# Kernel optimization log

Measured on AMD Instinct MI355X. Metric: run time of the kernel, lower is better.

## Reference

```python
import jax, jax.numpy as jnp
import numpy as np

B, T, D, H = 2048, 200, 128, 128


def setup_inputs() -> dict:
    key = jax.random.key(0)
    k1, k2, k3, k4, k5, k6 = jax.random.split(key, 6)
    inputs = jax.random.normal(k1, (B, T, D), dtype=jnp.float32)
    att_scores = jax.random.uniform(k2, (B, T), dtype=jnp.float32)
    seq_len = jax.random.randint(k3, (B,), 0, T, dtype=jnp.int32)
    s = 1.0 / np.sqrt(D + H)
    Wg = jax.random.normal(k4, (D + H, 2 * H), dtype=jnp.float32) * s
    bg = jnp.ones((2 * H,), dtype=jnp.float32)  # TF GRU gate bias init = 1.0
    Wc = jax.random.normal(k5, (D + H, H), dtype=jnp.float32) * s
    bc = jnp.zeros((H,), dtype=jnp.float32)
    return {"inputs": inputs, "att_scores": att_scores, "seq_len": seq_len,
            "Wg": Wg, "bg": bg, "Wc": Wc, "bc": bc}


def _augru_scan(inputs, att_scores, seq_len, Wg, bg, Wc, bc):
    # time-major xs for scan
    xs = (jnp.swapaxes(inputs, 0, 1),          # [T, B, D]
          jnp.swapaxes(att_scores, 0, 1),      # [T, B]
          jnp.arange(T, dtype=jnp.int32))      # [T]
    h0 = jnp.zeros((inputs.shape[0], H), dtype=inputs.dtype)

    def step(h, x):
        x_t, a_t, t = x
        # gates: sigmoid([x, h] @ Wg + bg) -> reset r, update u
        gi = jax.nn.sigmoid(jnp.concatenate([x_t, h], axis=-1) @ Wg + bg)
        r, u = jnp.split(gi, 2, axis=-1)
        # candidate: tanh([x, r*h] @ Wc + bc)
        c = jnp.tanh(jnp.concatenate([x_t, r * h], axis=-1) @ Wc + bc)
        # attention-gated update (AUGRU): scale update gate by att score
        u = a_t[:, None] * u
        new_h = (1.0 - u) * h + u * c
        # sequence-length masking (TF _rnn_step copy_cond: time >= seq_len)
        valid = (t < seq_len)[:, None]
        out = jnp.where(valid, new_h, jnp.zeros_like(new_h))  # zero_output
        h = jnp.where(valid, new_h, h)                         # carry old state
        return h, out

    final_h, outs = jax.lax.scan(step, h0, xs)
    return jnp.swapaxes(outs, 0, 1)  # [B, T, H]


def reference(inputs, att_scores, seq_len, Wg, bg, Wc, bc):
    return _augru_scan(inputs, att_scores, seq_len, Wg, bg, Wc, bc)
```

## Files before the change

### kernel.cpp

```cpp
#include <hip/hip_runtime.h>
#include <hip/hip_bf16.h>


#define BB   2048
#define TT   200
#define DD   128
#define HH   128
#define NG   256
#define BM   8
#define SB   136
#define SF   132
#define NTH  512

typedef __attribute__((ext_vector_type(8))) __bf16 bf16x8;
typedef __attribute__((ext_vector_type(4))) float  f32x4;

#define MFMA(a, b, c) __builtin_amdgcn_mfma_f32_16x16x32_bf16((a), (b), (c), 0, 0, 0)

union bfu { __bf16 b; unsigned short u; };
__device__ __forceinline__ unsigned short f2bf(float f) { bfu c; c.b = (__bf16)f; return c.u; }
__device__ __forceinline__ __bf16 f2bfv(float f) { return (__bf16)f; }

__device__ __forceinline__ void lds_barrier() {
    __builtin_amdgcn_sched_barrier(0);
    asm volatile("s_waitcnt lgkmcnt(0)" ::: "memory");
    __builtin_amdgcn_s_barrier();
    __builtin_amdgcn_sched_barrier(0);
}

__global__ __launch_bounds__(NTH, 2)
void augru_kernel(const float* __restrict__ X,
                  const float* __restrict__ ATT,
                  const int*   __restrict__ SL,
                  const float* __restrict__ WG,
                  const float* __restrict__ BG,
                  const float* __restrict__ WC,
                  const float* __restrict__ BC,
                  float*       __restrict__ OUT)
{
    __shared__ unsigned short xb[2][16 * SB];
    __shared__ unsigned short hb[16 * SB];
    __shared__ unsigned short rh[16 * SB];
    __shared__ float hs[BM * SF];
    __shared__ float ub[BM * SF];
    __shared__ float attall[BM * TT];
    __shared__ int   slbuf[BM];

    const int tid  = threadIdx.x;
    const int wave = tid >> 6;
    const int lane = tid & 63;
    const int quad = lane >> 4;
    const int l16  = lane & 15;
    const int b0   = blockIdx.x * BM;
    const int qq   = quad & 1;
    const int top  = quad >> 1;
    const int r0   = 4 * qq + 2 * top;

    for (int i = tid; i < 2 * 16 * SB; i += NTH) xb[0][i] = 0;
    for (int i = tid; i < 16 * SB; i += NTH) hb[i] = 0;
    for (int i = tid; i < 16 * SB; i += NTH) rh[i] = 0;
    for (int i = tid; i < BM * SF; i += NTH) { hs[i] = 0.f; ub[i] = 0.f; }
    for (int i = tid; i < BM * TT; i += NTH) attall[i] = ATT[(long)b0 * TT + i];
    if (tid < BM) slbuf[tid] = SL[b0 + tid];

    const float bgv0 = BG[(2 * wave) * 16 + l16];
    const float bgv1 = BG[(2 * wave + 1) * 16 + l16];
    const float bcv  = BC[wave * 16 + l16];

    bf16x8 bgf[2][8], bcf[8];
    {
        const int nc0 = (2 * wave) * 16 + l16;
        const int nc1 = nc0 + 16;
        const int ncc = wave * 16 + l16;
        #pragma unroll
        for (int kk = 0; kk < 8; ++kk) {
            bf16x8 t0, t1, t2;
            #pragma unroll
            for (int j = 0; j < 8; ++j) {
                const int k = kk * 32 + quad * 8 + j;
                t0[j] = f2bfv(WG[k * NG + nc0]);
                t1[j] = f2bfv(WG[k * NG + nc1]);
                t2[j] = f2bfv(WC[k * HH + ncc]);
            }
            bgf[0][kk] = t0; bgf[1][kk] = t1; bcf[kk] = t2;
        }
    }
    __syncthreads();

    int tmax = 0;
    #pragma unroll
    for (int r = 0; r < BM; ++r) tmax = max(tmax, slbuf[r]);
    const int sl0 = slbuf[r0], sl1 = slbuf[r0 + 1];

    const int srow = tid >> 5;
    const int sseg = tid & 31;

    float4 xpre;
    if (tid < 256 && tmax > 0) {
        xpre = *(const float4*)&X[((long)(b0 + srow) * TT + 0) * DD + sseg * 4];
        ushort4 v; v.x = f2bf(xpre.x); v.y = f2bf(xpre.y); v.z = f2bf(xpre.z); v.w = f2bf(xpre.w);
        *(ushort4*)&xb[0][srow * SB + sseg * 4] = v;
        if (tmax > 1)
            xpre = *(const float4*)&X[((long)(b0 + srow) * TT + 1) * DD + sseg * 4];
    }
    lds_barrier();

    for (int t = 0; t < tmax; ++t) {
        const unsigned short* xc = &xb[t & 1][0];

        bf16x8 afx[4];
        #pragma unroll
        for (int kk = 0; kk < 4; ++kk)
            afx[kk] = *(const bf16x8*)&xc[l16 * SB + kk * 32 + quad * 8];

        f32x4 a0 = {0.f,0.f,0.f,0.f}, a1 = {0.f,0.f,0.f,0.f};
        f32x4 a2 = {0.f,0.f,0.f,0.f}, a3 = {0.f,0.f,0.f,0.f};
        a0 = MFMA(afx[0], bgf[0][0], a0); a1 = MFMA(afx[0], bgf[1][0], a1);
        a2 = MFMA(afx[1], bgf[0][1], a2); a3 = MFMA(afx[1], bgf[1][1], a3);
        a0 = MFMA(afx[2], bgf[0][2], a0); a1 = MFMA(afx[2], bgf[1][2], a1);
        a2 = MFMA(afx[3], bgf[0][3], a2); a3 = MFMA(afx[3], bgf[1][3], a3);
        #pragma unroll
        for (int kk = 4; kk < 8; kk += 2) {
            const bf16x8 af0 = *(const bf16x8*)&hb[l16 * SB + (kk - 4) * 32 + quad * 8];
            const bf16x8 af1 = *(const bf16x8*)&hb[l16 * SB + (kk - 3) * 32 + quad * 8];
            a0 = MFMA(af0, bgf[0][kk], a0);     a1 = MFMA(af0, bgf[1][kk], a1);
            a2 = MFMA(af1, bgf[0][kk + 1], a2); a3 = MFMA(af1, bgf[1][kk + 1], a3);
        }

        if (tid < 256 && t + 1 < tmax) {
            ushort4 v; v.x = f2bf(xpre.x); v.y = f2bf(xpre.y); v.z = f2bf(xpre.z); v.w = f2bf(xpre.w);
            *(ushort4*)&xb[(t + 1) & 1][srow * SB + sseg * 4] = v;
            if (t + 2 < tmax)
                xpre = *(const float4*)&X[((long)(b0 + srow) * TT + (t + 2)) * DD + sseg * 4];
        }

        const f32x4 g0 = a0 + a2;
        const f32x4 g1 = a1 + a3;
        float s20 = __shfl_xor(g0[2], 32, 64), s30 = __shfl_xor(g0[3], 32, 64);
        float s21 = __shfl_xor(g1[2], 32, 64), s31 = __shfl_xor(g1[3], 32, 64);
        #pragma unroll
        for (int nt = 0; nt < 2; ++nt) {
            const int colg = (2 * wave + nt) * 16 + l16;
            const float bg = nt ? bgv1 : bgv0;
            const float v0 = top ? (nt ? s21 : s20) : (nt ? g1[0] : g0[0]);
            const float v1 = top ? (nt ? s31 : s30) : (nt ? g1[1] : g0[1]);
            #pragma unroll
            for (int rr = 0; rr < 2; ++rr) {
                const int row = r0 + rr;
                const float pre = (rr ? v1 : v0) + bg;
                const float s = __builtin_amdgcn_rcpf(1.0f + __expf(-pre));
                if (wave < 4) {
                    rh[row * SB + colg] = f2bf(s * hs[row * SF + colg]);
                } else {
                    ub[row * SF + (colg - HH)] = attall[row * TT + t] * s;
                }
            }
        }
        lds_barrier();

        f32x4 c0 = {0.f,0.f,0.f,0.f}, c1 = {0.f,0.f,0.f,0.f};
        f32x4 c2 = {0.f,0.f,0.f,0.f}, c3 = {0.f,0.f,0.f,0.f};
        {
            const bf16x8 afr0 = *(const bf16x8*)&rh[l16 * SB + 0 * 32 + quad * 8];
            const bf16x8 afr1 = *(const bf16x8*)&rh[l16 * SB + 1 * 32 + quad * 8];
            const bf16x8 afr2 = *(const bf16x8*)&rh[l16 * SB + 2 * 32 + quad * 8];
            const bf16x8 afr3 = *(const bf16x8*)&rh[l16 * SB + 3 * 32 + quad * 8];
            c0 = MFMA(afx[0], bcf[0], c0); c1 = MFMA(afr0, bcf[4], c1);
            c2 = MFMA(afx[1], bcf[1], c2); c3 = MFMA(afr1, bcf[5], c3);
            c0 = MFMA(afx[2], bcf[2], c0); c1 = MFMA(afr2, bcf[6], c1);
            c2 = MFMA(afx[3], bcf[3], c2); c3 = MFMA(afr3, bcf[7], c3);
        }
        const f32x4 cc = (c0 + c2) + (c1 + c3);
        float t2 = __shfl_xor(cc[2], 32, 64), t3 = __shfl_xor(cc[3], 32, 64);

        {
            const int col = wave * 16 + l16;
            const float w0 = top ? t2 : cc[0];
            const float w1 = top ? t3 : cc[1];
            #pragma unroll
            for (int rr = 0; rr < 2; ++rr) {
                const int row = r0 + rr;
                const float xv = (rr ? w1 : w0) + bcv;
                const float e  = __expf(2.0f * xv);
                const float c  = 1.0f - 2.0f * __builtin_amdgcn_rcpf(e + 1.0f);
                const float u  = ub[row * SF + col];
                const float ho = hs[row * SF + col];
                const float nh = fmaf(u, c - ho, ho);
                const bool valid = t < (rr ? sl1 : sl0);
                const float hst = valid ? nh : ho;
                hs[row * SF + col] = hst;
                hb[row * SB + col] = f2bf(hst);
                OUT[((long)(b0 + row) * TT + t) * HH + col] = valid ? nh : 0.f;
            }
        }
        lds_barrier();
    }

    const int n4 = (TT - tmax) * (HH / 4);
    for (int r = 0; r < BM; ++r) {
        float4* p = (float4*)(OUT + ((long)(b0 + r) * TT + tmax) * HH);
        for (int i = tid; i < n4; i += NTH) p[i] = make_float4(0.f, 0.f, 0.f, 0.f);
    }
}

extern "C" void kernel_launch(void* const* d_in, const int* in_sizes, int n_in,
                              void* d_out, int out_size, void* d_ws, size_t ws_size,
                              hipStream_t stream) {
    (void)in_sizes; (void)n_in; (void)d_ws; (void)ws_size; (void)out_size;
    const float* X   = (const float*)d_in[0];
    const float* ATT = (const float*)d_in[1];
    const int*   SL  = (const int*)d_in[2];
    const float* WG  = (const float*)d_in[3];
    const float* BG  = (const float*)d_in[4];
    const float* WC  = (const float*)d_in[5];
    const float* BC  = (const float*)d_in[6];
    float*       OUT = (float*)d_out;
    hipLaunchKernelGGL(augru_kernel, dim3(BB / BM), dim3(NTH), 0, stream,
                       X, ATT, SL, WG, BG, WC, BC, OUT);
}
```

Before: 573.8 us.

## Halve block to four waves, keep hidden state and update gate in registers

The block shrinks from 8 to 4 waves. Each wave now computes both the reset and update gate columns, plus two candidate column tiles, for the same 32 hidden columns. This lets the fp32 hidden state and the attention-scaled update gate stay in registers, removing the hs/ub shared-memory round trips and their loads and stores each step. The cost is double the register-resident weight fragments per thread, a launch bound of 1 block per SIMD slot, and more serial MFMA work per wave on the recurrent critical path.

```diff
diff --git a/kernel.cpp b/kernel.cpp
--- a/kernel.cpp
+++ b/kernel.cpp
@@ -9,8 +9,7 @@
 #define NG   256
 #define BM   8
 #define SB   136
-#define SF   132
-#define NTH  512
+#define NTH  256
 
 typedef __attribute__((ext_vector_type(8))) __bf16 bf16x8;
 typedef __attribute__((ext_vector_type(4))) float  f32x4;
@@ -20,6 +19,7 @@
 union bfu { __bf16 b; unsigned short u; };
 __device__ __forceinline__ unsigned short f2bf(float f) { bfu c; c.b = (__bf16)f; return c.u; }
 __device__ __forceinline__ __bf16 f2bfv(float f) { return (__bf16)f; }
+__device__ __forceinline__ float sigm(float x) { return __builtin_amdgcn_rcpf(1.0f + __expf(-x)); }
 
 __device__ __forceinline__ void lds_barrier() {
     __builtin_amdgcn_sched_barrier(0);
@@ -28,7 +28,7 @@
     __builtin_amdgcn_sched_barrier(0);
 }
 
-__global__ __launch_bounds__(NTH, 2)
+__global__ __launch_bounds__(NTH, 1)
 void augru_kernel(const float* __restrict__ X,
                   const float* __restrict__ ATT,
                   const int*   __restrict__ SL,
@@ -41,8 +41,6 @@
     __shared__ unsigned short xb[2][16 * SB];
     __shared__ unsigned short hb[16 * SB];
     __shared__ unsigned short rh[16 * SB];
-    __shared__ float hs[BM * SF];
-    __shared__ float ub[BM * SF];
     __shared__ float attall[BM * TT];
     __shared__ int   slbuf[BM];
 
@@ -59,30 +57,32 @@
     for (int i = tid; i < 2 * 16 * SB; i += NTH) xb[0][i] = 0;
     for (int i = tid; i < 16 * SB; i += NTH) hb[i] = 0;
     for (int i = tid; i < 16 * SB; i += NTH) rh[i] = 0;
-    for (int i = tid; i < BM * SF; i += NTH) { hs[i] = 0.f; ub[i] = 0.f; }
     for (int i = tid; i < BM * TT; i += NTH) attall[i] = ATT[(long)b0 * TT + i];
     if (tid < BM) slbuf[tid] = SL[b0 + tid];
 
-    const float bgv0 = BG[(2 * wave) * 16 + l16];
-    const float bgv1 = BG[(2 * wave + 1) * 16 + l16];
-    const float bcv  = BC[wave * 16 + l16];
-
-    bf16x8 bgf[2][8], bcf[8];
+    const int c0 = wave * 32 + l16;
+    const int c1 = c0 + 16;
+    const float bgr0 = BG[c0],      bgr1 = BG[c1];
+    const float bgu0 = BG[c0 + HH], bgu1 = BG[c1 + HH];
+    const float bc0v = BC[c0],      bc1v = BC[c1];
+
+    bf16x8 bgf[4][8], bcf[2][8];
     {
-        const int nc0 = (2 * wave) * 16 + l16;
-        const int nc1 = nc0 + 16;
-        const int ncc = wave * 16 + l16;
         #pragma unroll
         for (int kk = 0; kk < 8; ++kk) {
-            bf16x8 t0, t1, t2;
+            bf16x8 t0, t1, t2, t3, t4, t5;
             #pragma unroll
             for (int j = 0; j < 8; ++j) {
                 const int k = kk * 32 + quad * 8 + j;
-                t0[j] = f2bfv(WG[k * NG + nc0]);
-                t1[j] = f2bfv(WG[k * NG + nc1]);
-                t2[j] = f2bfv(WC[k * HH + ncc]);
-            }
-            bgf[0][kk] = t0; bgf[1][kk] = t1; bcf[kk] = t2;
+                t0[j] = f2bfv(WG[k * NG + c0]);
+                t1[j] = f2bfv(WG[k * NG + c1]);
+                t2[j] = f2bfv(WG[k * NG + c0 + HH]);
+                t3[j] = f2bfv(WG[k * NG + c1 + HH]);
+                t4[j] = f2bfv(WC[k * HH + c0]);
+                t5[j] = f2bfv(WC[k * HH + c1]);
+            }
+            bgf[0][kk] = t0; bgf[1][kk] = t1; bgf[2][kk] = t2; bgf[3][kk] = t3;
+            bcf[0][kk] = t4; bcf[1][kk] = t5;
         }
     }
     __syncthreads();
@@ -92,11 +92,13 @@
     for (int r = 0; r < BM; ++r) tmax = max(tmax, slbuf[r]);
     const int sl0 = slbuf[r0], sl1 = slbuf[r0 + 1];
 
+    float h00 = 0.f, h01 = 0.f, h10 = 0.f, h11 = 0.f;
+
     const int srow = tid >> 5;
     const int sseg = tid & 31;
 
     float4 xpre;
-    if (tid < 256 && tmax > 0) {
+    if (tmax > 0) {
         xpre = *(const float4*)&X[((long)(b0 + srow) * TT + 0) * DD + sseg * 4];
         ushort4 v; v.x = f2bf(xpre.x); v.y = f2bf(xpre.y); v.z = f2bf(xpre.z); v.w = f2bf(xpre.w);
         *(ushort4*)&xb[0][srow * SB + sseg * 4] = v;
@@ -113,84 +115,127 @@
         for (int kk = 0; kk < 4; ++kk)
             afx[kk] = *(const bf16x8*)&xc[l16 * SB + kk * 32 + quad * 8];
 
+        const float at0 = attall[r0 * TT + t];
+        const float at1 = attall[(r0 + 1) * TT + t];
+
         f32x4 a0 = {0.f,0.f,0.f,0.f}, a1 = {0.f,0.f,0.f,0.f};
         f32x4 a2 = {0.f,0.f,0.f,0.f}, a3 = {0.f,0.f,0.f,0.f};
-        a0 = MFMA(afx[0], bgf[0][0], a0); a1 = MFMA(afx[0], bgf[1][0], a1);
-        a2 = MFMA(afx[1], bgf[0][1], a2); a3 = MFMA(afx[1], bgf[1][1], a3);
-        a0 = MFMA(afx[2], bgf[0][2], a0); a1 = MFMA(afx[2], bgf[1][2], a1);
-        a2 = MFMA(afx[3], bgf[0][3], a2); a3 = MFMA(afx[3], bgf[1][3], a3);
-        #pragma unroll
-        for (int kk = 4; kk < 8; kk += 2) {
-            const bf16x8 af0 = *(const bf16x8*)&hb[l16 * SB + (kk - 4) * 32 + quad * 8];
-            const bf16x8 af1 = *(const bf16x8*)&hb[l16 * SB + (kk - 3) * 32 + quad * 8];
-            a0 = MFMA(af0, bgf[0][kk], a0);     a1 = MFMA(af0, bgf[1][kk], a1);
-            a2 = MFMA(af1, bgf[0][kk + 1], a2); a3 = MFMA(af1, bgf[1][kk + 1], a3);
-        }
-
-        if (tid < 256 && t + 1 < tmax) {
+        f32x4 a4 = {0.f,0.f,0.f,0.f}, a5 = {0.f,0.f,0.f,0.f};
+        f32x4 a6 = {0.f,0.f,0.f,0.f}, a7 = {0.f,0.f,0.f,0.f};
+        a0 = MFMA(afx[0], bgf[0][0], a0); a2 = MFMA(afx[0], bgf[1][0], a2);
+        a4 = MFMA(afx[0], bgf[2][0], a4); a6 = MFMA(afx[0], bgf[3][0], a6);
+        a1 = MFMA(afx[1], bgf[0][1], a1); a3 = MFMA(afx[1], bgf[1][1], a3);
+        a5 = MFMA(afx[1], bgf[2][1], a5); a7 = MFMA(afx[1], bgf[3][1], a7);
+        a0 = MFMA(afx[2], bgf[0][2], a0); a2 = MFMA(afx[2], bgf[1][2], a2);
+        a4 = MFMA(afx[2], bgf[2][2], a4); a6 = MFMA(afx[2], bgf[3][2], a6);
+        a1 = MFMA(afx[3], bgf[0][3], a1); a3 = MFMA(afx[3], bgf[1][3], a3);
+        a5 = MFMA(afx[3], bgf[2][3], a5); a7 = MFMA(afx[3], bgf[3][3], a7);
+        {
+            const bf16x8 afh0 = *(const bf16x8*)&hb[l16 * SB + 0 * 32 + quad * 8];
+            const bf16x8 afh1 = *(const bf16x8*)&hb[l16 * SB + 1 * 32 + quad * 8];
+            const bf16x8 afh2 = *(const bf16x8*)&hb[l16 * SB + 2 * 32 + quad * 8];
+            const bf16x8 afh3 = *(const bf16x8*)&hb[l16 * SB + 3 * 32 + quad * 8];
+            a0 = MFMA(afh0, bgf[0][4], a0); a2 = MFMA(afh0, bgf[1][4], a2);
+            a4 = MFMA(afh0, bgf[2][4], a4); a6 = MFMA(afh0, bgf[3][4], a6);
+            a1 = MFMA(afh1, bgf[0][5], a1); a3 = MFMA(afh1, bgf[1][5], a3);
+            a5 = MFMA(afh1, bgf[2][5], a5); a7 = MFMA(afh1, bgf[3][5], a7);
+            a0 = MFMA(afh2, bgf[0][6], a0); a2 = MFMA(afh2, bgf[1][6], a2);
+            a4 = MFMA(afh2, bgf[2][6], a4); a6 = MFMA(afh2, bgf[3][6], a6);
+            a1 = MFMA(afh3, bgf[0][7], a1); a3 = MFMA(afh3, bgf[1][7], a3);
+            a5 = MFMA(afh3, bgf[2][7], a5); a7 = MFMA(afh3, bgf[3][7], a7);
+        }
+
+        if (t + 1 < tmax) {
             ushort4 v; v.x = f2bf(xpre.x); v.y = f2bf(xpre.y); v.z = f2bf(xpre.z); v.w = f2bf(xpre.w);
             *(ushort4*)&xb[(t + 1) & 1][srow * SB + sseg * 4] = v;
             if (t + 2 < tmax)
                 xpre = *(const float4*)&X[((long)(b0 + srow) * TT + (t + 2)) * DD + sseg * 4];
         }
 
-        const f32x4 g0 = a0 + a2;
-        const f32x4 g1 = a1 + a3;
-        float s20 = __shfl_xor(g0[2], 32, 64), s30 = __shfl_xor(g0[3], 32, 64);
-        float s21 = __shfl_xor(g1[2], 32, 64), s31 = __shfl_xor(g1[3], 32, 64);
-        #pragma unroll
-        for (int nt = 0; nt < 2; ++nt) {
-            const int colg = (2 * wave + nt) * 16 + l16;
-            const float bg = nt ? bgv1 : bgv0;
-            const float v0 = top ? (nt ? s21 : s20) : (nt ? g1[0] : g0[0]);
-            const float v1 = top ? (nt ? s31 : s30) : (nt ? g1[1] : g0[1]);
-            #pragma unroll
-            for (int rr = 0; rr < 2; ++rr) {
-                const int row = r0 + rr;
-                const float pre = (rr ? v1 : v0) + bg;
-                const float s = __builtin_amdgcn_rcpf(1.0f + __expf(-pre));
-                if (wave < 4) {
-                    rh[row * SB + colg] = f2bf(s * hs[row * SF + colg]);
-                } else {
-                    ub[row * SF + (colg - HH)] = attall[row * TT + t] * s;
-                }
-            }
+        const f32x4 gr0 = a0 + a1;
+        const f32x4 gr1 = a2 + a3;
+        const f32x4 gu0 = a4 + a5;
+        const f32x4 gu1 = a6 + a7;
+        const float r02 = __shfl_xor(gr0[2], 32, 64), r03 = __shfl_xor(gr0[3], 32, 64);
+        const float r12 = __shfl_xor(gr1[2], 32, 64), r13 = __shfl_xor(gr1[3], 32, 64);
+        const float u02 = __shfl_xor(gu0[2], 32, 64), u03 = __shfl_xor(gu0[3], 32, 64);
+        const float u12 = __shfl_xor(gu1[2], 32, 64), u13 = __shfl_xor(gu1[3], 32, 64);
+        float ug00, ug01, ug10, ug11;
+        {
+            const float rs00 = sigm((top ? r02 : gr0[0]) + bgr0);
+            const float rs10 = sigm((top ? r03 : gr0[1]) + bgr0);
+            rh[r0 * SB + c0]       = f2bf(rs00 * h00);
+            rh[(r0 + 1) * SB + c0] = f2bf(rs10 * h10);
+            ug00 = at0 * sigm((top ? u02 : gu0[0]) + bgu0);
+            ug10 = at1 * sigm((top ? u03 : gu0[1]) + bgu0);
+            const float rs01 = sigm((top ? r12 : gr1[0]) + bgr1);
+            const float rs11 = sigm((top ? r13 : gr1[1]) + bgr1);
+            rh[r0 * SB + c1]       = f2bf(rs01 * h01);
+            rh[(r0 + 1) * SB + c1] = f2bf(rs11 * h11);
+            ug01 = at0 * sigm((top ? u12 : gu1[0]) + bgu1);
+            ug11 = at1 * sigm((top ? u13 : gu1[1]) + bgu1);
         }
         lds_barrier();
 
-        f32x4 c0 = {0.f,0.f,0.f,0.f}, c1 = {0.f,0.f,0.f,0.f};
-        f32x4 c2 = {0.f,0.f,0.f,0.f}, c3 = {0.f,0.f,0.f,0.f};
+        f32x4 q0 = {0.f,0.f,0.f,0.f}, q1 = {0.f,0.f,0.f,0.f};
+        f32x4 q2 = {0.f,0.f,0.f,0.f}, q3 = {0.f,0.f,0.f,0.f};
         {
             const bf16x8 afr0 = *(const bf16x8*)&rh[l16 * SB + 0 * 32 + quad * 8];
             const bf16x8 afr1 = *(const bf16x8*)&rh[l16 * SB + 1 * 32 + quad * 8];
             const bf16x8 afr2 = *(const bf16x8*)&rh[l16 * SB + 2 * 32 + quad * 8];
             const bf16x8 afr3 = *(const bf16x8*)&rh[l16 * SB + 3 * 32 + quad * 8];
-            c0 = MFMA(afx[0], bcf[0], c0); c1 = MFMA(afr0, bcf[4], c1);
-            c2 = MFMA(afx[1], bcf[1], c2); c3 = MFMA(afr1, bcf[5], c3);
-            c0 = MFMA(afx[2], bcf[2], c0); c1 = MFMA(afr2, bcf[6], c1);
-            c2 = MFMA(afx[3], bcf[3], c2); c3 = MFMA(afr3, bcf[7], c3);
-        }
-        const f32x4 cc = (c0 + c2) + (c1 + c3);
-        float t2 = __shfl_xor(cc[2], 32, 64), t3 = __shfl_xor(cc[3], 32, 64);
-
-        {
-            const int col = wave * 16 + l16;
-            const float w0 = top ? t2 : cc[0];
-            const float w1 = top ? t3 : cc[1];
-            #pragma unroll
-            for (int rr = 0; rr < 2; ++rr) {
-                const int row = r0 + rr;
-                const float xv = (rr ? w1 : w0) + bcv;
-                const float e  = __expf(2.0f * xv);
-                const float c  = 1.0f - 2.0f * __builtin_amdgcn_rcpf(e + 1.0f);
-                const float u  = ub[row * SF + col];
-                const float ho = hs[row * SF + col];
-                const float nh = fmaf(u, c - ho, ho);
-                const bool valid = t < (rr ? sl1 : sl0);
-                const float hst = valid ? nh : ho;
-                hs[row * SF + col] = hst;
-                hb[row * SB + col] = f2bf(hst);
-                OUT[((long)(b0 + row) * TT + t) * HH + col] = valid ? nh : 0.f;
+            q0 = MFMA(afx[0], bcf[0][0], q0); q2 = MFMA(afx[0], bcf[1][0], q2);
+            q1 = MFMA(afx[1], bcf[0][1], q1); q3 = MFMA(afx[1], bcf[1][1], q3);
+            q0 = MFMA(afx[2], bcf[0][2], q0); q2 = MFMA(afx[2], bcf[1][2], q2);
+            q1 = MFMA(afx[3], bcf[0][3], q1); q3 = MFMA(afx[3], bcf[1][3], q3);
+            q0 = MFMA(afr0, bcf[0][4], q0);   q2 = MFMA(afr0, bcf[1][4], q2);
+            q1 = MFMA(afr1, bcf[0][5], q1);   q3 = MFMA(afr1, bcf[1][5], q3);
+            q0 = MFMA(afr2, bcf[0][6], q0);   q2 = MFMA(afr2, bcf[1][6], q2);
+            q1 = MFMA(afr3, bcf[0][7], q1);   q3 = MFMA(afr3, bcf[1][7], q3);
+        }
+        const f32x4 cc0 = q0 + q1;
+        const f32x4 cc1 = q2 + q3;
+        const float c02 = __shfl_xor(cc0[2], 32, 64), c03 = __shfl_xor(cc0[3], 32, 64);
+        const float c12 = __shfl_xor(cc1[2], 32, 64), c13 = __shfl_xor(cc1[3], 32, 64);
+
+        {
+            const bool v0 = t < sl0;
+            const bool v1 = t < sl1;
+            {
+                const float xv = (top ? c02 : cc0[0]) + bc0v;
+                const float e  = __expf(2.0f * xv);
+                const float cd = 1.0f - 2.0f * __builtin_amdgcn_rcpf(e + 1.0f);
+                const float nh = fmaf(ug00, cd - h00, h00);
+                h00 = v0 ? nh : h00;
+                hb[r0 * SB + c0] = f2bf(h00);
+                OUT[((long)(b0 + r0) * TT + t) * HH + c0] = v0 ? nh : 0.f;
+            }
+            {
+                const float xv = (top ? c03 : cc0[1]) + bc0v;
+                const float e  = __expf(2.0f * xv);
+                const float cd = 1.0f - 2.0f * __builtin_amdgcn_rcpf(e + 1.0f);
+                const float nh = fmaf(ug10, cd - h10, h10);
+                h10 = v1 ? nh : h10;
+                hb[(r0 + 1) * SB + c0] = f2bf(h10);
+                OUT[((long)(b0 + r0 + 1) * TT + t) * HH + c0] = v1 ? nh : 0.f;
+            }
+            {
+                const float xv = (top ? c12 : cc1[0]) + bc1v;
+                const float e  = __expf(2.0f * xv);
+                const float cd = 1.0f - 2.0f * __builtin_amdgcn_rcpf(e + 1.0f);
+                const float nh = fmaf(ug01, cd - h01, h01);
+                h01 = v0 ? nh : h01;
+                hb[r0 * SB + c1] = f2bf(h01);
+                OUT[((long)(b0 + r0) * TT + t) * HH + c1] = v0 ? nh : 0.f;
+            }
+            {
+                const float xv = (top ? c13 : cc1[1]) + bc1v;
+                const float e  = __expf(2.0f * xv);
+                const float cd = 1.0f - 2.0f * __builtin_amdgcn_rcpf(e + 1.0f);
+                const float nh = fmaf(ug11, cd - h11, h11);
+                h11 = v1 ? nh : h11;
+                hb[(r0 + 1) * SB + c1] = f2bf(h11);
+                OUT[((long)(b0 + r0 + 1) * TT + t) * HH + c1] = v1 ? nh : 0.f;
             }
         }
         lds_barrier();
```

Result: faster. 501.2 us, median of 2 (-12.7%).
